# Optimization experiments

Hardware: AMD Instinct MI355X
Metric: run time of the kernel (lower is better)

The kernel has to match this reference:

```python
import jax, jax.numpy as jnp
import numpy as np

H = 16          # n_self_heads
CHUNK = 256     # chunk_size in chunk_gate_retention
GLN = 16.0      # gate_logit_normalizer
EPS = 1e-5      # norm_eps


def _rope_interleaved(t, cos, sin):
    # t: [B,T,H,hd]; cos,sin: [T,hd//2]; interleaved pairs (even, odd)
    x1 = t[..., 0::2]
    x2 = t[..., 1::2]
    c = cos[None, :, None, :]
    s = sin[None, :, None, :]
    r1 = x1 * c - x2 * s
    r2 = x1 * s + x2 * c
    return jnp.stack([r1, r2], axis=-1).reshape(t.shape)


def setup_inputs() -> dict:
    key = jax.random.key(0)
    ks = jax.random.split(key, 8)
    B, T, D = 2, 4096, 2048
    hd = D // H
    sc = D ** -0.5
    x = jax.random.normal(ks[0], (B, T, D), jnp.float32)
    # real rotary tables (interleaved), [T, hd//2]
    inv_freq = 1.0 / (10000.0 ** (np.arange(0, hd, 2, dtype=np.float32) / hd))
    ang = np.outer(np.arange(T, dtype=np.float32), inv_freq)
    cos = jnp.asarray(np.cos(ang))
    sin = jnp.asarray(np.sin(ang))
    Wq = jax.random.normal(ks[1], (D, D), jnp.float32) * sc
    Wk = jax.random.normal(ks[2], (D, D), jnp.float32) * sc
    Wv = jax.random.normal(ks[3], (D, D), jnp.float32) * sc
    Wg = jax.random.normal(ks[4], (D, D), jnp.float32) * sc
    Wgt = jax.random.normal(ks[5], (D, H), jnp.float32) * sc
    Wout = jax.random.normal(ks[6], (D, D), jnp.float32) * sc
    return {"x": x, "cos": cos, "sin": sin, "Wq": Wq, "Wk": Wk, "Wv": Wv,
            "Wg": Wg, "Wgt": Wgt, "Wout": Wout}


def reference(x, cos, sin, Wq, Wk, Wv, Wg, Wgt, Wout):
    B, T, D = x.shape
    hd = D // H
    N = T // CHUNK
    scale = hd ** -0.5

    q = (x @ Wq).reshape(B, T, H, hd)
    k = (x @ Wk).reshape(B, T, H, hd)
    v = (x @ Wv).reshape(B, T, H, hd)
    g = x @ Wg                                   # [B,T,D] swiglu gate
    gt = jax.nn.log_sigmoid(x @ Wgt) / GLN       # [B,T,H] log-decay per head

    q = _rope_interleaved(q, cos, sin)
    k = _rope_interleaved(k, cos, sin)

    # chunk: [B,H,N,C,hd]
    def chunked(t):
        return t.transpose(0, 2, 1, 3).reshape(B, H, N, CHUNK, hd)
    qc, kc, vc = chunked(q), chunked(k), chunked(v)

    gtc = gt.transpose(0, 2, 1).reshape(B, H, N, CHUNK).astype(jnp.float32)
    gcum = jnp.cumsum(gtc, axis=-1)              # inclusive cumsum within chunk

    # intra-chunk: A[i,j] = (q_i.k_j)*scale * exp(gcum_i - gcum_j), j <= i
    mask = jnp.tril(jnp.ones((CHUNK, CHUNK), bool))
    dec = jnp.where(mask, jnp.exp(gcum[..., :, None] - gcum[..., None, :]), 0.0).astype(x.dtype)
    scores = jnp.einsum('bhncd,bhnsd->bhncs', qc * scale, kc) * dec
    o_inner = jnp.einsum('bhncs,bhnsd->bhncd', scores, vc)

    # cross-chunk recurrent state: S <- S*exp(g_total) + (k*exp(g_total-gcum))^T V * scale
    g_tot = gcum[..., -1:]                       # [B,H,N,1]
    k_dec = jnp.exp(g_tot - gcum).astype(x.dtype)
    S_in = jnp.einsum('bhncd,bhnce->bhnde', kc * k_dec[..., None] * scale, vc)  # [B,H,N,hd,hd]
    q_dec = jnp.exp(gcum).astype(x.dtype)        # [B,H,N,C]
    chunk_dec = jnp.exp(gcum[..., -1]).astype(x.dtype)  # [B,H,N]

    def step(S, inp):
        qcn, qd, Sin, cd = inp
        o_cross = jnp.einsum('bhcd,bhde->bhce', qcn * qd[..., None], S)
        S_new = S * cd[..., None, None] + Sin
        return S_new, o_cross

    xs = (jnp.moveaxis(qc, 2, 0), jnp.moveaxis(q_dec, 2, 0),
          jnp.moveaxis(S_in, 2, 0), jnp.moveaxis(chunk_dec, 2, 0))
    S0 = jnp.zeros((B, H, hd, hd), x.dtype)
    _, o_cross = jax.lax.scan(step, S0, xs)      # [N,B,H,C,hd]

    o = o_inner + jnp.moveaxis(o_cross, 0, 2)    # [B,H,N,C,hd]
    # RMSNorm over head_dim, no affine
    o = o * jax.lax.rsqrt(jnp.mean(o * o, axis=-1, keepdims=True) + EPS)
    o = o.reshape(B, H, T, hd).transpose(0, 2, 1, 3).reshape(B, T, D)
    o = jax.nn.silu(g) * o                       # swiglu(g, o)
    return o @ Wout
```

## Files before the change

kernel.cpp:

```cpp
#include <hip/hip_runtime.h>

typedef unsigned short u16;
typedef short bf16x8 __attribute__((ext_vector_type(8)));
typedef unsigned short u16x8 __attribute__((ext_vector_type(8)));
typedef unsigned short u16x4 __attribute__((ext_vector_type(4)));
typedef float f32x4 __attribute__((ext_vector_type(4)));

typedef __attribute__((address_space(1))) void* gas_ptr;
typedef __attribute__((address_space(3))) void* las_ptr;

__device__ __forceinline__ float bf2f(u16 v) {
  unsigned u = ((unsigned)v) << 16;
  return __builtin_bit_cast(float, u);
}
__device__ __forceinline__ u16 f2bf(float f) {
  unsigned u = __builtin_bit_cast(unsigned, f);
  u += 0x7fffu + ((u >> 16) & 1u);
  return (u16)(u >> 16);
}
__device__ __forceinline__ f32x4 mfma16(bf16x8 a, bf16x8 b, f32x4 c) {
  return __builtin_amdgcn_mfma_f32_16x16x32_bf16(a, b, c, 0, 0, 0);
}
__device__ __forceinline__ void gload_lds16(const void* g, void* l) {
  __builtin_amdgcn_global_load_lds((gas_ptr)g, (las_ptr)l, 16, 0, 0);
}

#define SB __builtin_amdgcn_sched_barrier(0)
#define BAR do { SB; __builtin_amdgcn_s_barrier(); SB; } while (0)

__global__ void k_cast(const float* __restrict__ in, u16* __restrict__ out, int n8) {
  int stride = gridDim.x * blockDim.x;
  for (int i = blockIdx.x * blockDim.x + threadIdx.x; i < n8; i += stride) {
    size_t base = (size_t)i * 8;
    f32x4 a = *(const f32x4*)(in + base);
    f32x4 b = *(const f32x4*)(in + base + 4);
    u16x8 o;
    o[0] = f2bf(a[0]); o[1] = f2bf(a[1]); o[2] = f2bf(a[2]); o[3] = f2bf(a[3]);
    o[4] = f2bf(b[0]); o[5] = f2bf(b[1]); o[6] = f2bf(b[2]); o[7] = f2bf(b[3]);
    *(u16x8*)(out + base) = o;
  }
}

__global__ __launch_bounds__(256) void k_wtrans5(const float* __restrict__ W0,
                                                 const float* __restrict__ W1,
                                                 const float* __restrict__ W2,
                                                 const float* __restrict__ W3,
                                                 const float* __restrict__ W4,
                                                 u16* __restrict__ WT) {
  const int K = 2048, N = 2048;
  int z = blockIdx.z;
  const float* W = (z == 0) ? W0 : (z == 1) ? W1 : (z == 2) ? W2 : (z == 3) ? W3 : W4;
  u16* dst = WT + (size_t)z * 4194304;
  int n0 = blockIdx.x * 64, k0 = blockIdx.y * 64;
  int tid = threadIdx.x;
  __shared__ __align__(16) float tf[64][68];
  int r = tid >> 4, c4 = (tid & 15) * 4;
#pragma unroll
  for (int i = 0; i < 4; ++i) {
    int row = r + i * 16;
    f32x4 v = *(const f32x4*)(W + (size_t)(k0 + row) * N + n0 + c4);
    *(f32x4*)&tf[row][c4] = v;
  }
  __syncthreads();
#pragma unroll
  for (int i = 0; i < 2; ++i) {
    int chunk = tid + i * 256;
    int nl = chunk >> 3, c8 = (chunk & 7) * 8;
    u16x8 o;
#pragma unroll
    for (int m = 0; m < 8; ++m) o[m] = f2bf(tf[c8 + m][nl]);
    *(u16x8*)(dst + (size_t)(n0 + nl) * K + k0 + c8) = o;
  }
}

template <int MODE>
__global__ __launch_bounds__(512, 2) void k_gemm2(const u16* __restrict__ A,
                                                  const u16* __restrict__ Bt,
                                                  void* __restrict__ Cp, int M, int N, int K) {
  __shared__ __align__(16) u16 Al[2][2][8192];
  __shared__ __align__(16) u16 Bl[2][2][8192];
  int tid = threadIdx.x, w = tid >> 6, lane = tid & 63, l15 = lane & 15, l4 = lane >> 4;
  int wm = w >> 2, wn = w & 3;
  int nwg = gridDim.x, bid = blockIdx.x;
  int q8 = nwg >> 3;
  int wg = (bid & 7) * q8 + (bid >> 3);
  int nbx = N >> 8;
  int nstx = nbx >> 2;
  int st = wg >> 4, r16 = wg & 15;
  int sm = st / nstx, sn = st - sm * nstx;
  int m0 = ((sm << 2) + (r16 >> 2)) << 8;
  int n0 = ((sn << 2) + (r16 & 3)) << 8;
  int rA0, rA1, rB0, rB1, cc0, cc1;
  {
    int rr[2], cch[2];
#pragma unroll
    for (int q = 0; q < 2; ++q) {
      int L = (q * 512 + tid) * 16;
      int sub = L >> 10, inner = L & 1023;
      inner ^= ((inner >> 9) & 1) << 5;
      rr[q] = ((sub >> 1) << 4) + (inner >> 6);
      cch[q] = ((sub & 1) << 5) + ((inner & 63) >> 1);
    }
    rA0 = ((rr[0] >> 6) << 7) + (rr[0] & 63);
    rA1 = ((rr[1] >> 6) << 7) + (rr[1] & 63);
    rB0 = ((rr[0] >> 5) << 6) + (rr[0] & 31);
    rB1 = ((rr[1] >> 5) << 6) + (rr[1] & 31);
    cc0 = cch[0]; cc1 = cch[1];
  }
  int innerA = ((l15 << 6) + (l4 << 4)) ^ ((l15 & 8) << 2);
  int ldsW = w << 9;

#define STAGE_A(t, h)                                                                   \
  do {                                                                                  \
    int b_ = (t) & 1;                                                                   \
    gload_lds16(A + (size_t)(m0 + rA0 + (h) * 64) * K + (t) * 64 + cc0, &Al[b_][h][ldsW]); \
    gload_lds16(A + (size_t)(m0 + rA1 + (h) * 64) * K + (t) * 64 + cc1, &Al[b_][h][4096 + ldsW]); \
  } while (0)
#define STAGE_B(t, h)                                                                   \
  do {                                                                                  \
    int b_ = (t) & 1;                                                                   \
    gload_lds16(Bt + (size_t)(n0 + rB0 + (h) * 32) * K + (t) * 64 + cc0, &Bl[b_][h][ldsW]); \
    gload_lds16(Bt + (size_t)(n0 + rB1 + (h) * 32) * K + (t) * 64 + cc1, &Bl[b_][h][4096 + ldsW]); \
  } while (0)

  const f32x4 z4 = {0.f, 0.f, 0.f, 0.f};
  f32x4 acc[8][4];
#pragma unroll
  for (int i = 0; i < 8; ++i)
#pragma unroll
    for (int j = 0; j < 4; ++j) acc[i][j] = z4;
  bf16x8 af0[4][2], af1[4][2], bf0[2][2], bf1[2][2];

#define LDA_H(AF, buf, hh, fi0, fi1)                                                     \
  do {                                                                                   \
    const char* Ab = (const char*)&Al[buf][hh][0];                                       \
    _Pragma("unroll") for (int fi = (fi0); fi < (fi1); ++fi)                             \
        _Pragma("unroll") for (int ks = 0; ks < 2; ++ks)                                 \
            AF[fi][ks] = *(const bf16x8*)(Ab + (((wm * 4 + fi) * 2 + ks) << 10) + innerA); \
  } while (0)
#define LDB_H(BF, buf, hh)                                                               \
  do {                                                                                   \
    const char* Bb = (const char*)&Bl[buf][hh][0];                                       \
    _Pragma("unroll") for (int fj = 0; fj < 2; ++fj)                                     \
        _Pragma("unroll") for (int ks = 0; ks < 2; ++ks)                                 \
            BF[fj][ks] = *(const bf16x8*)(Bb + (((wn * 2 + fj) * 2 + ks) << 10) + innerA); \
  } while (0)
#define MM(hm, hn, AF, BF)                                                               \
  do {                                                                                   \
    __builtin_amdgcn_s_setprio(1);                                                       \
    _Pragma("unroll") for (int fi = 0; fi < 4; ++fi) _Pragma("unroll") for (int fj = 0; fj < 2; ++fj) \
        _Pragma("unroll") for (int ks = 0; ks < 2; ++ks)                                 \
            acc[(hm) * 4 + fi][(hn) * 2 + fj] =                                          \
                mfma16(AF[fi][ks], BF[fj][ks], acc[(hm) * 4 + fi][(hn) * 2 + fj]);       \
    __builtin_amdgcn_s_setprio(0);                                                       \
  } while (0)

  int nt = K >> 6;
  STAGE_A(0, 0); STAGE_B(0, 0); STAGE_B(0, 1); STAGE_A(0, 1);
  if (nt > 1) {
    STAGE_A(1, 0); STAGE_B(1, 0);
    asm volatile("s_waitcnt vmcnt(4)" ::: "memory");
  } else {
    asm volatile("s_waitcnt vmcnt(0)" ::: "memory");
  }
  SB;
  BAR;
  LDA_H(af0, 0, 0, 0, 2); LDA_H(af0, 0, 0, 2, 4); LDB_H(bf0, 0, 0);
  for (int t = 0; t < nt; ++t) {
    int cur = t & 1, nxt = cur ^ 1;
    LDB_H(bf1, cur, 1); LDA_H(af1, cur, 1, 0, 2);
    if (t + 1 < nt) STAGE_B(t + 1, 1);
    asm volatile("s_waitcnt lgkmcnt(8)" ::: "memory"); SB;
    MM(0, 0, af0, bf0);
    BAR;
    LDA_H(af1, cur, 1, 2, 4);
    if (t + 1 < nt) STAGE_A(t + 1, 1);
    asm volatile("s_waitcnt lgkmcnt(8)" ::: "memory"); SB;
    MM(0, 1, af0, bf1);
    if (t + 1 < nt) { asm volatile("s_waitcnt vmcnt(4)" ::: "memory"); }
    else            { asm volatile("s_waitcnt vmcnt(0)" ::: "memory"); }
    SB;
    BAR;
    if (t + 1 < nt) LDA_H(af0, nxt, 0, 0, 2);
    if (t + 2 < nt) STAGE_A(t + 2, 0);
    if (t + 1 < nt) { asm volatile("s_waitcnt lgkmcnt(4)" ::: "memory"); }
    else            { asm volatile("s_waitcnt lgkmcnt(0)" ::: "memory"); }
    SB;
    MM(1, 0, af1, bf0);
    BAR;
    if (t + 1 < nt) { LDA_H(af0, nxt, 0, 2, 4); LDB_H(bf0, nxt, 0); }
    if (t + 2 < nt) STAGE_B(t + 2, 0);
    MM(1, 1, af1, bf1);
    BAR;
  }
  asm volatile("s_waitcnt lgkmcnt(0)" ::: "memory");
  asm volatile("s_waitcnt vmcnt(0)" ::: "memory");
#undef STAGE_A
#undef STAGE_B
#undef LDA_H
#undef LDB_H
#undef MM
#pragma unroll
  for (int fi = 0; fi < 8; ++fi)
#pragma unroll
    for (int fj = 0; fj < 4; ++fj) {
      int row = m0 + wm * 128 + fi * 16 + l4 * 4;
      int col = n0 + wn * 64 + fj * 16 + l15;
      if (MODE == 1) {
        float* C = (float*)Cp;
#pragma unroll
        for (int reg = 0; reg < 4; ++reg) C[(size_t)(row + reg) * N + col] = acc[fi][fj][reg];
      } else {
        u16* C = (u16*)Cp + (size_t)(col >> 11) * 16777216 + (col & 2047);
#pragma unroll
        for (int reg = 0; reg < 4; ++reg) C[(size_t)(row + reg) * 2048] = f2bf(acc[fi][fj][reg]);
      }
    }
}

__global__ __launch_bounds__(256) void k_gt(const float* __restrict__ x, const float* __restrict__ Wgt,
                                            float* __restrict__ gt) {
  int t = blockIdx.x, tid = threadIdx.x;
  __shared__ __align__(16) float xs[2048];
#pragma unroll
  for (int i = 0; i < 8; ++i) xs[tid + i * 256] = x[(size_t)t * 2048 + tid + i * 256];
  __syncthreads();
  int head = tid & 15, ks = tid >> 4;
  float p = 0.f;
  for (int i = 0; i < 128; ++i) {
    int k = ks + i * 16;
    p += xs[k] * Wgt[k * 16 + head];
  }
  __shared__ float ps[16][17];
  ps[ks][head] = p;
  __syncthreads();
  if (tid < 16) {
    float z = 0.f;
#pragma unroll
    for (int j = 0; j < 16; ++j) z += ps[j][tid];
    float lsz = (z >= 0.f) ? -log1pf(__expf(-z)) : (z - log1pf(__expf(z)));
    int b = t >> 12, tl = t & 4095;
    gt[((size_t)(b * 16 + tid)) * 4096 + tl] = lsz * 0.0625f;
  }
}

__global__ void k_cumsum(const float* __restrict__ gt, float* __restrict__ gcum) {
  int n = blockIdx.x, bh = blockIdx.y, c = threadIdx.x;
  __shared__ float s[256];
  size_t base = (size_t)bh * 4096 + n * 256;
  s[c] = gt[base + c];
  __syncthreads();
  for (int off = 1; off < 256; off <<= 1) {
    float t = (c >= off) ? s[c - off] : 0.f;
    __syncthreads();
    s[c] += t;
    __syncthreads();
  }
  gcum[base + c] = s[c];
}

__global__ void k_rope(u16* __restrict__ q, u16* __restrict__ k,
                       const float* __restrict__ cosT, const float* __restrict__ sinT) {
  const size_t total = (size_t)8192 * 512;
  size_t stride = (size_t)gridDim.x * blockDim.x;
  for (size_t idx = (size_t)blockIdx.x * blockDim.x + threadIdx.x; idx < total; idx += stride) {
    size_t tok = idx >> 9;
    int g4 = (int)(idx & 511);
    int col = g4 * 4;
    int i0 = (col & 127) >> 1;
    int tl = (int)(tok & 4095);
    float c0 = cosT[tl * 64 + i0], s0 = sinT[tl * 64 + i0];
    float c1 = cosT[tl * 64 + i0 + 1], s1 = sinT[tl * 64 + i0 + 1];
    size_t base = tok * 2048 + col;
    u16x4 qv = *(u16x4*)(q + base);
    float a0 = bf2f(qv[0]), a1 = bf2f(qv[1]), a2 = bf2f(qv[2]), a3 = bf2f(qv[3]);
    u16x4 qo;
    qo[0] = f2bf(a0 * c0 - a1 * s0); qo[1] = f2bf(a0 * s0 + a1 * c0);
    qo[2] = f2bf(a2 * c1 - a3 * s1); qo[3] = f2bf(a2 * s1 + a3 * c1);
    *(u16x4*)(q + base) = qo;
    u16x4 kv = *(u16x4*)(k + base);
    float b0 = bf2f(kv[0]), b1 = bf2f(kv[1]), b2 = bf2f(kv[2]), b3 = bf2f(kv[3]);
    u16x4 ko;
    ko[0] = f2bf(b0 * c0 - b1 * s0); ko[1] = f2bf(b0 * s0 + b1 * c0);
    ko[2] = f2bf(b2 * c1 - b3 * s1); ko[3] = f2bf(b2 * s1 + b3 * c1);
    *(u16x4*)(k + base) = ko;
  }
}

__global__ __launch_bounds__(256) void k_sin(const u16* __restrict__ kb, const u16* __restrict__ vb,
                                             const float* __restrict__ gcum, float* __restrict__ SinT) {
  int n = blockIdx.x, bh = blockIdx.y;
  int b = bh >> 4, h = bh & 15;
  int tid = threadIdx.x, w = tid >> 6, lane = tid & 63, l15 = lane & 15, l4 = lane >> 4;
  size_t t0 = (size_t)b * 4096 + n * 256;
  __shared__ float gc[256];
  __shared__ __align__(16) u16 kt[128 * 72];
  __shared__ __align__(16) u16 vt[128 * 72];
  gc[tid] = gcum[(size_t)bh * 4096 + n * 256 + tid];
  __syncthreads();
  float gtot = gc[255];
  const float scale = 0.08838834764831845f;
  const f32x4 z4 = {0.f, 0.f, 0.f, 0.f};
  f32x4 acc[2][8];
#pragma unroll
  for (int i = 0; i < 2; ++i)
#pragma unroll
    for (int j = 0; j < 8; ++j) acc[i][j] = z4;
  int cl = tid >> 2, fq = (tid & 3) * 32;
  for (int c0 = 0; c0 < 256; c0 += 64) {
    __syncthreads();
    float kd = __expf(gtot - gc[c0 + cl]) * scale;
    const u16* kp = kb + (t0 + c0 + cl) * 2048 + h * 128 + fq;
    const u16* vp = vb + (t0 + c0 + cl) * 2048 + h * 128 + fq;
#pragma unroll
    for (int jj = 0; jj < 4; ++jj) {
      u16x8 kv = *(const u16x8*)(kp + jj * 8);
      u16x8 vv = *(const u16x8*)(vp + jj * 8);
#pragma unroll
      for (int m = 0; m < 8; ++m) {
        int f = fq + jj * 8 + m;
        kt[f * 72 + cl] = f2bf(bf2f(kv[m]) * kd);
        vt[f * 72 + cl] = vv[m];
      }
    }
    __syncthreads();
#pragma unroll
    for (int ks = 0; ks < 2; ++ks) {
      int coff = ks * 32 + l4 * 8;
      bf16x8 bfr[8];
#pragma unroll
      for (int bc = 0; bc < 8; ++bc) bfr[bc] = *(const bf16x8*)(vt + (bc * 16 + l15) * 72 + coff);
#pragma unroll
      for (int ar = 0; ar < 2; ++ar) {
        bf16x8 afr = *(const bf16x8*)(kt + (w * 32 + ar * 16 + l15) * 72 + coff);
#pragma unroll
        for (int bc = 0; bc < 8; ++bc) acc[ar][bc] = mfma16(afr, bfr[bc], acc[ar][bc]);
      }
    }
  }
  size_t sbo = ((size_t)bh * 16 + n) * 16384;
#pragma unroll
  for (int ar = 0; ar < 2; ++ar) {
    int d = w * 32 + ar * 16 + l4 * 4;
#pragma unroll
    for (int bc = 0; bc < 8; ++bc) {
      int e = bc * 16 + l15;
      *(f32x4*)(SinT + sbo + (size_t)e * 128 + d) = acc[ar][bc];
    }
  }
}

__global__ void k_state(const float* __restrict__ SinT, const float* __restrict__ gcum,
                        u16* __restrict__ S_T) {
  int bh = blockIdx.x >> 3, sl = blockIdx.x & 7;
  int base_l = sl * 2048 + threadIdx.x;
  float S[8];
#pragma unroll
  for (int i = 0; i < 8; ++i) S[i] = 0.f;
  for (int nn = 0; nn < 16; ++nn) {
    size_t tb = ((size_t)bh * 16 + nn) * 16384;
#pragma unroll
    for (int i = 0; i < 8; ++i) S_T[tb + base_l + i * 256] = f2bf(S[i]);
    float cd = __expf(gcum[(size_t)bh * 4096 + nn * 256 + 255]);
#pragma unroll
    for (int i = 0; i < 8; ++i) S[i] = S[i] * cd + SinT[tb + base_l + i * 256];
  }
}

__global__ __launch_bounds__(512, 4) void k_attn(
    const u16* __restrict__ qb, const u16* __restrict__ kb, const u16* __restrict__ vb,
    const u16* __restrict__ gbuf, const float* __restrict__ gcum,
    const u16* __restrict__ S_T, u16* __restrict__ ob) {
  int n = blockIdx.x, bh = blockIdx.y;
  int b = bh >> 4, h = bh & 15;
  int tid = threadIdx.x, w = tid >> 6, lane = tid & 63, l15 = lane & 15, l4 = lane >> 4;
  size_t t0 = (size_t)b * 4096 + n * 256;
  __shared__ float gc[256];
  __shared__ __align__(16) u16 vt[32768];
  __shared__ __align__(16) u16 Pb[8][512];
  if (tid < 256) gc[tid] = gcum[(size_t)bh * 4096 + n * 256 + tid];
  {
    int s = tid & 255, e0 = (tid >> 8) * 64;
    const u16* vp = vb + (t0 + s) * 2048 + h * 128 + e0;
#pragma unroll
    for (int j = 0; j < 8; ++j) {
      u16x8 vv = *(const u16x8*)(vp + j * 8);
#pragma unroll
      for (int m = 0; m < 8; ++m) {
        int e = e0 + j * 8 + m;
        vt[(e * 256 + s) ^ ((e & 7) << 3)] = vv[m];
      }
    }
  }
  __syncthreads();
  const float scale = 0.08838834764831845f;
  u16* P = Pb[w];
  const f32x4 z4 = {0.f, 0.f, 0.f, 0.f};
  f32x4 acc[2][8];
#pragma unroll
  for (int i = 0; i < 2; ++i)
#pragma unroll
    for (int j = 0; j < 8; ++j) acc[i][j] = z4;
  int r0s[2], nsbs[2];
  r0s[0] = w * 16;        nsbs[0] = (w + 2) >> 1;
  r0s[1] = (15 - w) * 16; nsbs[1] = 8 - (w >> 1);
#pragma unroll
  for (int rb = 0; rb < 2; ++rb) {
    int r0 = r0s[rb], nsb = nsbs[rb];
    bf16x8 qa[4];
    {
      const u16* qp = qb + (t0 + r0 + l15) * 2048 + h * 128 + l4 * 8;
#pragma unroll
      for (int ks = 0; ks < 4; ++ks) qa[ks] = *(const bf16x8*)(qp + ks * 32);
    }
    for (int sbk = 0; sbk < nsb; ++sbk) {
      int s0 = sbk * 32;
      f32x4 sc[2] = {z4, z4};
#pragma unroll
      for (int cf = 0; cf < 2; ++cf) {
        const u16* kp = kb + (t0 + s0 + cf * 16 + l15) * 2048 + h * 128 + l4 * 8;
#pragma unroll
        for (int ks = 0; ks < 4; ++ks)
          sc[cf] = mfma16(qa[ks], *(const bf16x8*)(kp + ks * 32), sc[cf]);
      }
#pragma unroll
      for (int cf = 0; cf < 2; ++cf) {
        int s = s0 + cf * 16 + l15;
        float gs = gc[s];
#pragma unroll
        for (int reg = 0; reg < 4; ++reg) {
          int rl = l4 * 4 + reg;
          int r = r0 + rl;
          float val = (r >= s) ? sc[cf][reg] * scale * __expf(gc[r] - gs) : 0.f;
          P[(rl * 32 + cf * 16 + l15) ^ ((rl & 3) << 3)] = f2bf(val);
        }
      }
      bf16x8 pa = *(const bf16x8*)(P + ((l15 * 32 + l4 * 8) ^ ((l15 & 3) << 3)));
#pragma unroll
      for (int bc = 0; bc < 8; ++bc) {
        int e = bc * 16 + l15;
        bf16x8 vf = *(const bf16x8*)(vt + ((e * 256 + s0 + l4 * 8) ^ ((e & 7) << 3)));
        acc[rb][bc] = mfma16(pa, vf, acc[rb][bc]);
      }
    }
  }
  size_t sbase = ((size_t)bh * 16 + n) * 16384;
#pragma unroll
  for (int rb = 0; rb < 2; ++rb) {
    int r0 = r0s[rb];
    float qd = __expf(gc[r0 + l15]);
#pragma unroll
    for (int ks = 0; ks < 4; ++ks) {
      u16x8 qu = *(const u16x8*)(qb + (t0 + r0 + l15) * 2048 + h * 128 + ks * 32 + l4 * 8);
      u16x8 ru;
#pragma unroll
      for (int m = 0; m < 8; ++m) ru[m] = f2bf(bf2f(qu[m]) * qd);
      bf16x8 pa2 = __builtin_bit_cast(bf16x8, ru);
#pragma unroll
      for (int bc = 0; bc < 8; ++bc) {
        int e = bc * 16 + l15;
        bf16x8 sf = *(const bf16x8*)(S_T + sbase + (size_t)e * 128 + ks * 32 + l4 * 8);
        acc[rb][bc] = mfma16(pa2, sf, acc[rb][bc]);
      }
    }
  }
#pragma unroll
  for (int rb = 0; rb < 2; ++rb) {
    int r0 = r0s[rb];
#pragma unroll
    for (int reg = 0; reg < 4; ++reg) {
      float ss = 0.f;
#pragma unroll
      for (int bc = 0; bc < 8; ++bc) { float v = acc[rb][bc][reg]; ss += v * v; }
      ss += __shfl_xor(ss, 1);
      ss += __shfl_xor(ss, 2);
      ss += __shfl_xor(ss, 4);
      ss += __shfl_xor(ss, 8);
      float rinv = rsqrtf(ss * 0.0078125f + 1e-5f);
      int r = r0 + l4 * 4 + reg;
      size_t rowoff = (t0 + r) * 2048 + h * 128;
#pragma unroll
      for (int bc = 0; bc < 8; ++bc) {
        int e = bc * 16 + l15;
        float gval = bf2f(gbuf[rowoff + e]);
        float sig = 1.f / (1.f + __expf(-gval));
        ob[rowoff + e] = f2bf(acc[rb][bc][reg] * rinv * gval * sig);
      }
    }
  }
}

extern "C" void kernel_launch(void* const* d_in, const int* in_sizes, int n_in,
                              void* d_out, int out_size, void* d_ws, size_t ws_size,
                              hipStream_t stream) {
  const float* x    = (const float*)d_in[0];
  const float* cosT = (const float*)d_in[1];
  const float* sinT = (const float*)d_in[2];
  const float* Wq   = (const float*)d_in[3];
  const float* Wk   = (const float*)d_in[4];
  const float* Wv   = (const float*)d_in[5];
  const float* Wg   = (const float*)d_in[6];
  const float* Wgt  = (const float*)d_in[7];
  const float* Wout = (const float*)d_in[8];
  float* out = (float*)d_out;

  const size_t MB32 = (size_t)33554432;
  const size_t W8   = (size_t)8388608;
  char* ws = (char*)d_ws;
  size_t need = MB32 + 5 * W8 + 4 * MB32 + 2 * (size_t)524288;
  if (ws_size < need) return;

  u16*   xb    = (u16*)(ws);
  float* SinT  = (float*)(ws);
  u16*   ob    = (u16*)(ws);
  u16*   WqT   = (u16*)(ws + MB32);
  u16*   S_T   = (u16*)(ws + MB32);
  u16*   WoutT = (u16*)(ws + MB32 + 4 * W8);
  u16*   qb    = (u16*)(ws + MB32 + 5 * W8);
  u16*   kb    = qb + 16777216;
  u16*   vb    = qb + 2 * 16777216;
  u16*   gb    = qb + 3 * (size_t)16777216;
  float* gt    = (float*)(ws + MB32 + 5 * W8 + 4 * MB32);
  float* gcum  = (float*)(ws + MB32 + 5 * W8 + 4 * MB32 + 524288);

  k_cast<<<2048, 256, 0, stream>>>(x, xb, 2097152);
  k_wtrans5<<<dim3(32, 32, 5), 256, 0, stream>>>(Wq, Wk, Wv, Wg, Wout, WqT);

  k_gemm2<2><<<1024, 512, 0, stream>>>(xb, WqT, qb, 8192, 8192, 2048);

  k_gt<<<8192, 256, 0, stream>>>(x, Wgt, gt);
  k_cumsum<<<dim3(16, 32), 256, 0, stream>>>(gt, gcum);
  k_rope<<<4096, 256, 0, stream>>>(qb, kb, cosT, sinT);
  k_sin<<<dim3(16, 32), 256, 0, stream>>>(kb, vb, gcum, SinT);
  k_state<<<256, 256, 0, stream>>>(SinT, gcum, S_T);
  k_attn<<<dim3(16, 32), 512, 0, stream>>>(qb, kb, vb, gb, gcum, S_T, ob);
  k_gemm2<1><<<256, 512, 0, stream>>>(ob, WoutT, out, 8192, 2048, 2048);
}
```

Before: 548.6 us.

## Simplify GEMM main loop schedule, drop sched barriers and manual lgkmcnt waits

Restructures the bf16 GEMM main loop so that each quadrant's A/B fragments are loaded from LDS just before use, rather than prefetching the next tile's fragments across iterations. It removes the sched_barrier fences and explicit lgkmcnt waits and leaves that scheduling to the compiler. It also reorders the prologue staging and moves the vmcnt wait to the end of each iteration. This may cut register pressure and simplify the code, but it gives up the hand-tuned overlap of LDS reads with MFMA work. The compiler may also serialize or misplace waits around the barriers.

```diff
diff --git a/kernel.cpp b/kernel.cpp
--- a/kernel.cpp
+++ b/kernel.cpp
@@ -24,9 +24,6 @@
 __device__ __forceinline__ void gload_lds16(const void* g, void* l) {
   __builtin_amdgcn_global_load_lds((gas_ptr)g, (las_ptr)l, 16, 0, 0);
 }
-
-#define SB __builtin_amdgcn_sched_barrier(0)
-#define BAR do { SB; __builtin_amdgcn_s_barrier(); SB; } while (0)
 
 __global__ void k_cast(const float* __restrict__ in, u16* __restrict__ out, int n8) {
   int stride = gridDim.x * blockDim.x;
@@ -131,10 +128,10 @@
     for (int j = 0; j < 4; ++j) acc[i][j] = z4;
   bf16x8 af0[4][2], af1[4][2], bf0[2][2], bf1[2][2];
 
-#define LDA_H(AF, buf, hh, fi0, fi1)                                                     \
+#define LDA_H(AF, buf, hh)                                                               \
   do {                                                                                   \
     const char* Ab = (const char*)&Al[buf][hh][0];                                       \
-    _Pragma("unroll") for (int fi = (fi0); fi < (fi1); ++fi)                             \
+    _Pragma("unroll") for (int fi = 0; fi < 4; ++fi)                                     \
         _Pragma("unroll") for (int ks = 0; ks < 2; ++ks)                                 \
             AF[fi][ks] = *(const bf16x8*)(Ab + (((wm * 4 + fi) * 2 + ks) << 10) + innerA); \
   } while (0)
@@ -156,44 +153,39 @@
   } while (0)
 
   int nt = K >> 6;
-  STAGE_A(0, 0); STAGE_B(0, 0); STAGE_B(0, 1); STAGE_A(0, 1);
+  STAGE_A(0, 0); STAGE_B(0, 0); STAGE_A(0, 1); STAGE_B(0, 1);
   if (nt > 1) {
     STAGE_A(1, 0); STAGE_B(1, 0);
     asm volatile("s_waitcnt vmcnt(4)" ::: "memory");
   } else {
     asm volatile("s_waitcnt vmcnt(0)" ::: "memory");
   }
-  SB;
-  BAR;
-  LDA_H(af0, 0, 0, 0, 2); LDA_H(af0, 0, 0, 2, 4); LDB_H(bf0, 0, 0);
+  __builtin_amdgcn_s_barrier();
   for (int t = 0; t < nt; ++t) {
-    int cur = t & 1, nxt = cur ^ 1;
-    LDB_H(bf1, cur, 1); LDA_H(af1, cur, 1, 0, 2);
+    int cur = t & 1;
+    LDA_H(af0, cur, 0); LDB_H(bf0, cur, 0);
+    if (t + 1 < nt) STAGE_A(t + 1, 1);
+    __builtin_amdgcn_s_barrier();
+    MM(0, 0, af0, bf0);
+    __builtin_amdgcn_s_barrier();
+    LDB_H(bf1, cur, 1);
     if (t + 1 < nt) STAGE_B(t + 1, 1);
-    asm volatile("s_waitcnt lgkmcnt(8)" ::: "memory"); SB;
-    MM(0, 0, af0, bf0);
-    BAR;
-    LDA_H(af1, cur, 1, 2, 4);
-    if (t + 1 < nt) STAGE_A(t + 1, 1);
-    asm volatile("s_waitcnt lgkmcnt(8)" ::: "memory"); SB;
+    __builtin_amdgcn_s_barrier();
     MM(0, 1, af0, bf1);
-    if (t + 1 < nt) { asm volatile("s_waitcnt vmcnt(4)" ::: "memory"); }
-    else            { asm volatile("s_waitcnt vmcnt(0)" ::: "memory"); }
-    SB;
-    BAR;
-    if (t + 1 < nt) LDA_H(af0, nxt, 0, 0, 2);
+    __builtin_amdgcn_s_barrier();
+    LDA_H(af1, cur, 1);
     if (t + 2 < nt) STAGE_A(t + 2, 0);
-    if (t + 1 < nt) { asm volatile("s_waitcnt lgkmcnt(4)" ::: "memory"); }
-    else            { asm volatile("s_waitcnt lgkmcnt(0)" ::: "memory"); }
-    SB;
+    __builtin_amdgcn_s_barrier();
     MM(1, 0, af1, bf0);
-    BAR;
-    if (t + 1 < nt) { LDA_H(af0, nxt, 0, 2, 4); LDB_H(bf0, nxt, 0); }
+    __builtin_amdgcn_s_barrier();
     if (t + 2 < nt) STAGE_B(t + 2, 0);
     MM(1, 1, af1, bf1);
-    BAR;
-  }
-  asm volatile("s_waitcnt lgkmcnt(0)" ::: "memory");
+    if (t + 1 < nt) {
+      if (t + 2 < nt) { asm volatile("s_waitcnt vmcnt(4)" ::: "memory"); }
+      else            { asm volatile("s_waitcnt vmcnt(0)" ::: "memory"); }
+    }
+    __builtin_amdgcn_s_barrier();
+  }
   asm volatile("s_waitcnt vmcnt(0)" ::: "memory");
 #undef STAGE_A
 #undef STAGE_B
```

Measured after the change: 561.9 us. 1.02x slower.
